# Performance work log

Measured on AMD Instinct MI355X. Metric: run time of the kernel, lower is better.

The kernel has to match this reference:

```python
import jax, jax.numpy as jnp
import numpy as np

SIGMA = 10.0
EPSILON = 46.0
BATCH = 4096
D_X = 1024
D_Y = 512


def setup_inputs() -> dict:
    key = jax.random.key(0)
    kx, ky = jax.random.split(key)
    x = jax.random.normal(kx, (BATCH, D_X), dtype=jnp.float32)
    y = jax.random.normal(ky, (BATCH, D_Y), dtype=jnp.float32)
    return {"x": x, "y": y}


def _pairwise_l2(a):
    # [B, B] matrix of ||a_i - a_j||_2 via the matmul trick; safe sqrt for grads.
    sq = jnp.sum(a * a, axis=-1)                      # [B]
    d2 = sq[:, None] + sq[None, :] - 2.0 * (a @ a.T)  # [B, B]
    d2 = jnp.maximum(d2, 0.0)
    return jnp.sqrt(jnp.where(d2 > 1e-12, d2, 1e-12))


def reference(x, y):
    b = x.shape[0]
    dx = _pairwise_l2(x)   # ||x_i - x_j||
    dy = _pairwise_l2(y)   # ||y_i - y_j||
    offdiag = 1.0 - jnp.eye(b, dtype=x.dtype)          # i != j
    mask = offdiag * (dx <= EPSILON).astype(x.dtype)   # threshold at epsilon
    w = jnp.exp(-dx / SIGMA)                           # heat-kernel weight
    loss = jnp.sum(mask * w * dy)
    return loss
```

## Files before the change

### kernel.cpp

```cpp
#include <hip/hip_runtime.h>
#include <hip/hip_bf16.h>
#include <hip/hip_fp8.h>
#include <stdint.h>

#define BATCH 4096
#define D_X   1024
#define D_Y   512

constexpr float SIGMA_INV = 0.1f;
constexpr float EPS_THR   = 46.0f;

constexpr int BMF   = 128;
constexpr int NTF   = BATCH / BMF;
constexpr int NBLKF = NTF * (NTF + 1) / 2;
constexpr int XS8   = D_X / 16;
constexpr int YS8   = D_Y / 16;

constexpr int BM = 128;
constexpr int NT = BATCH / BM;
constexpr int NBLK = NT * (NT + 1) / 2;

typedef __bf16 bf16x8 __attribute__((ext_vector_type(8)));
typedef float  f32x4  __attribute__((ext_vector_type(4)));
typedef unsigned short u16x8 __attribute__((ext_vector_type(8)));
typedef unsigned long long u64;
typedef u64 u64x2 __attribute__((ext_vector_type(2)));

__device__ __forceinline__ unsigned short f32_to_bf16_bits(float f) {
    unsigned int u = __builtin_bit_cast(unsigned int, f);
    unsigned int r = (u + 0x7FFFu + ((u >> 16) & 1u)) >> 16;
    return (unsigned short)r;
}

__device__ __forceinline__ int perm16(int u8) {
    int ks = u8 >> 2, kg = u8 & 3;
    return (ks >> 1) * 8 + kg * 2 + (ks & 1);
}

__global__ void __launch_bounds__(192)
convert_fp8(const float* __restrict__ x, const float* __restrict__ y,
            u64* __restrict__ xq, u64* __restrict__ yq,
            float* __restrict__ sqx, float* __restrict__ sqy) {
    __shared__ float part[2];
    const int row = blockIdx.x;
    const int t   = threadIdx.x;
    const int lane = t & 63;
    const int wid  = t >> 6;

    float nrm = 0.f;
    if (t < 128) {
        const float4* p = (const float4*)(x + (size_t)row * D_X + t * 8);
        float4 f0 = p[0], f1 = p[1];
        float e[8] = {f0.x, f0.y, f0.z, f0.w, f1.x, f1.y, f1.z, f1.w};
        u64 w = 0;
#pragma unroll
        for (int i = 0; i < 8; ++i) {
            __hip_fp8_e4m3 q(e[i]);
            float b = (float)q;
            nrm = fmaf(b, b, nrm);
            w |= (u64)q.__x << (8 * i);
        }
        xq[(size_t)row * 128 + (t & ~15) + perm16(t & 15)] = w;
    } else {
        int o = t - 128;
        const float4* p = (const float4*)(y + (size_t)row * D_Y + o * 8);
        float4 f0 = p[0], f1 = p[1];
        float e[8] = {f0.x, f0.y, f0.z, f0.w, f1.x, f1.y, f1.z, f1.w};
        u64 w = 0;
#pragma unroll
        for (int i = 0; i < 8; ++i) {
            __hip_fp8_e4m3 q(e[i]);
            float b = (float)q;
            nrm = fmaf(b, b, nrm);
            w |= (u64)q.__x << (8 * i);
        }
        yq[(size_t)row * 64 + (o & ~15) + perm16(o & 15)] = w;
    }
#pragma unroll
    for (int off = 32; off > 0; off >>= 1)
        nrm += __shfl_down(nrm, off, 64);
    if (lane == 0) {
        if (wid < 2) part[wid] = nrm;
        else         sqy[row] = nrm;
    }
    __syncthreads();
    if (t == 0) sqx[row] = part[0] + part[1];
}


__device__ __forceinline__ u64x2 ldsfrag2(const u16x8* T, int row, int c) {
    int slot = c ^ (row & 7);
    return __builtin_bit_cast(u64x2, T[row * 8 + slot]);
}

#define ISSUE(DST, BASE, OFF)                                              \
    {                                                                      \
        _Pragma("unroll")                                                  \
        for (int it = 0; it < 8; ++it)                                     \
            __builtin_amdgcn_global_load_lds(                              \
                (const uint32_t __attribute__((address_space(1)))*)(BASE[it] + (OFF)), \
                (uint32_t __attribute__((address_space(3)))*)((DST) + it * 256 + wid * 64), \
                16, 0, 0);                                                 \
    }

#define FRAGS_READ(BUF)                                                    \
        u64x2 fa[2][4], fb[2][4];                      \
        _Pragma("unroll")                                                  \
        for (int t2 = 0; t2 < 2; ++t2) {                                   \
            _Pragma("unroll")                                              \
            for (int m = 0; m < 4; ++m)                                    \
                fa[t2][m] = ldsfrag2(BUF, wr * 64 + m * 16 + lrow,         \
                                     t2 * 4 + kgrp);                       \
            _Pragma("unroll")                                              \
            for (int n = 0; n < 4; ++n)                                    \
                fb[t2][n] = ldsfrag2(BUF, 128 + wc * 64 + n * 16 + lrow,   \
                                     t2 * 4 + kgrp);                       \
        }

#define FRAGS_MFMA(ACC)                                                    \
        __builtin_amdgcn_s_setprio(1);                                     \
        _Pragma("unroll")                                                  \
        for (int t2 = 0; t2 < 2; ++t2)                                     \
            _Pragma("unroll")                                              \
            for (int h = 0; h < 2; ++h)                                    \
                _Pragma("unroll")                                          \
                for (int m = 0; m < 4; ++m)                                \
                    _Pragma("unroll")                                      \
                    for (int n = 0; n < 4; ++n)                            \
                        ACC[m][n] =                                        \
                            __builtin_amdgcn_mfma_f32_16x16x32_fp8_fp8(    \
                                (long)fa[t2][m][h], (long)fb[t2][n][h],    \
                                ACC[m][n], 0, 0, 0);                       \
        __builtin_amdgcn_s_setprio(0);

#define GSTEP(BUF, ACC, W, IBASE, IOFF)                                    \
    {                                                                      \
        asm volatile("s_waitcnt vmcnt(" #W ")" ::: "memory");              \
        __builtin_amdgcn_s_barrier();                                      \
        FRAGS_READ(BUF)                                                    \
        asm volatile("s_waitcnt lgkmcnt(0)" ::: "memory");                 \
        __builtin_amdgcn_s_barrier();                                      \
        ISSUE(BUF, IBASE, IOFF)                                            \
        FRAGS_MFMA(ACC)                                                    \
    }
#define GSTEP_NOISSUE(BUF, ACC, W)                                         \
    {                                                                      \
        asm volatile("s_waitcnt vmcnt(" #W ")" ::: "memory");              \
        __builtin_amdgcn_s_barrier();                                      \
        FRAGS_READ(BUF)                                                    \
        FRAGS_MFMA(ACC)                                                    \
    }

__global__ void __launch_bounds__(256, 2)
gram_fp8(const u16x8* __restrict__ xq, const u16x8* __restrict__ yq,
         const float* __restrict__ sqx, const float* __restrict__ sqy,
         float* __restrict__ out) {
    __shared__ u16x8 T0[2048], T1[2048];
    __shared__ float snxA[BMF], snxB[BMF], snyA[BMF], snyB[BMF];
    __shared__ float wsum[4];

    const int tid  = threadIdx.x;
    const int lane = tid & 63;
    const int wid  = tid >> 6;
    const int wr   = wid >> 1;
    const int wc   = wid & 1;
    const int lrow = lane & 15;
    const int kgrp = lane >> 4;

    int sb = (blockIdx.x & 7) * (NBLKF / 8) + (blockIdx.x >> 3);

    int t0 = sb, bi = 0;
    while (t0 >= NTF - bi) { t0 -= NTF - bi; ++bi; }
    const int bj = bi + t0;
    const int iA = bi * BMF;
    const int iB = bj * BMF;
    const bool diag = (bi == bj);

    if (tid < BMF) {
        snxA[tid] = sqx[iA + tid];
        snyA[tid] = sqy[iA + tid];
    } else {
        int u = tid - BMF;
        snxB[u] = sqx[iB + u];
        snyB[u] = sqy[iB + u];
    }

    const char* g[8];
#pragma unroll
    for (int it = 0; it < 8; ++it) {
        int ul   = it * 256 + wid * 64 + lane;
        int row  = ul >> 3;
        int st   = ul & 7;
        int lg   = st ^ (row & 7);
        int grow = (row < 128 ? iA + row : iB + row - 128);
        g[it] = (const char*)xq + (size_t)grow * (XS8 * 16) + lg * 16;
    }

    f32x4 accX[4][4] = {};
    f32x4 accY[4][4] = {};

    ISSUE(T0, g, 0)
    ISSUE(T1, g, 128)

    GSTEP(T0, accX, 8, g, 256)
    GSTEP(T1, accX, 8, g, 384)
    GSTEP(T0, accX, 8, g, 512)
    GSTEP(T1, accX, 8, g, 640)
    GSTEP(T0, accX, 8, g, 768)
    GSTEP(T1, accX, 8, g, 896)

#pragma unroll
    for (int it = 0; it < 8; ++it) {
        int ul   = it * 256 + wid * 64 + lane;
        int row  = ul >> 3;
        int st   = ul & 7;
        int lg   = st ^ (row & 7);
        int grow = (row < 128 ? iA + row : iB + row - 128);
        g[it] = (const char*)yq + (size_t)grow * (YS8 * 16) + lg * 16;
    }

    GSTEP(T0, accX, 8, g, 0)
    GSTEP(T1, accX, 8, g, 128)
    GSTEP(T0, accY, 8, g, 256)
    GSTEP(T1, accY, 8, g, 384)
    GSTEP_NOISSUE(T0, accY, 8)
    GSTEP_NOISSUE(T1, accY, 0)

    float local = 0.f;
#pragma unroll
    for (int m = 0; m < 4; ++m) {
#pragma unroll
        for (int n = 0; n < 4; ++n) {
            int col   = wc * 64 + n * 16 + lrow;
            float sxj = snxB[col];
            float syj = snyB[col];
#pragma unroll
            for (int r = 0; r < 4; ++r) {
                int rowi  = wr * 64 + m * 16 + kgrp * 4 + r;
                float d2x = snxA[rowi] + sxj - 2.f * accX[m][n][r];
                float dxv = sqrtf(fmaxf(d2x, 1e-12f));
                float d2y = snyA[rowi] + syj - 2.f * accY[m][n][r];
                float dyv = sqrtf(fmaxf(d2y, 1e-12f));
                int gi = iA + rowi, gj = iB + col;
                bool keep = (gi != gj) && (dxv <= EPS_THR);
                float contrib = __expf(-dxv * SIGMA_INV) * dyv;
                local += keep ? contrib : 0.f;
            }
        }
    }
    if (!diag) local *= 2.f;

#pragma unroll
    for (int off = 32; off > 0; off >>= 1)
        local += __shfl_down(local, off, 64);
    if (lane == 0) wsum[wid] = local;
    __syncthreads();
    if (tid == 0)
        atomicAdd(out, wsum[0] + wsum[1] + wsum[2] + wsum[3]);
}

__global__ void norms_kernel_fb(const float* __restrict__ x,
                                const float* __restrict__ y,
                                float* __restrict__ sqx,
                                float* __restrict__ sqy) {
    int row = blockIdx.x;
    int t   = threadIdx.x;
    const float4* xr = (const float4*)(x + (size_t)row * D_X);
    float sx = 0.f;
#pragma unroll
    for (int i = 0; i < D_X / 4 / 64; ++i) {
        float4 v = xr[t + i * 64];
        sx += v.x * v.x + v.y * v.y + v.z * v.z + v.w * v.w;
    }
    const float4* yr = (const float4*)(y + (size_t)row * D_Y);
    float sy = 0.f;
#pragma unroll
    for (int i = 0; i < D_Y / 4 / 64; ++i) {
        float4 v = yr[t + i * 64];
        sy += v.x * v.x + v.y * v.y + v.z * v.z + v.w * v.w;
    }
#pragma unroll
    for (int off = 32; off > 0; off >>= 1) {
        sx += __shfl_down(sx, off, 64);
        sy += __shfl_down(sy, off, 64);
    }
    if (t == 0) { sqx[row] = sx; sqy[row] = sy; }
}

__device__ __forceinline__ void stage_tile_fb(const float* __restrict__ src, int ld,
                                              int base_row, int k0,
                                              u16x8* __restrict__ dst, int tid) {
#pragma unroll
    for (int it = 0; it < 2; ++it) {
        int u   = tid + it * 256;
        int row = u >> 2;
        int q   = u & 3;
        const float4* p = (const float4*)(src + (size_t)(base_row + row) * ld + k0 + q * 16);
        float4 f0 = p[0], f1 = p[1], f2 = p[2], f3 = p[3];
        u16x8 lo, hi;
        lo[0] = f32_to_bf16_bits(f0.x); lo[1] = f32_to_bf16_bits(f0.y);
        lo[2] = f32_to_bf16_bits(f0.z); lo[3] = f32_to_bf16_bits(f0.w);
        lo[4] = f32_to_bf16_bits(f1.x); lo[5] = f32_to_bf16_bits(f1.y);
        lo[6] = f32_to_bf16_bits(f1.z); lo[7] = f32_to_bf16_bits(f1.w);
        hi[0] = f32_to_bf16_bits(f2.x); hi[1] = f32_to_bf16_bits(f2.y);
        hi[2] = f32_to_bf16_bits(f2.z); hi[3] = f32_to_bf16_bits(f2.w);
        hi[4] = f32_to_bf16_bits(f3.x); hi[5] = f32_to_bf16_bits(f3.y);
        hi[6] = f32_to_bf16_bits(f3.z); hi[7] = f32_to_bf16_bits(f3.w);
        int swz = row & 7;
        dst[row * 8 + ((2 * q) ^ swz)]     = lo;
        dst[row * 8 + ((2 * q + 1) ^ swz)] = hi;
    }
}

__device__ __forceinline__ void mfma16_fb(const bf16x8 a[4], const bf16x8 b[4],
                                          f32x4 acc[4][4]) {
#pragma unroll
    for (int m = 0; m < 4; ++m)
#pragma unroll
        for (int n = 0; n < 4; ++n)
            acc[m][n] = __builtin_amdgcn_mfma_f32_16x16x32_bf16(
                a[m], b[n], acc[m][n], 0, 0, 0);
}

__device__ __forceinline__ void load_frags_fb(const u16x8* As_, const u16x8* Bs_,
                                              int wr, int wc, int lrow, int kgrp,
                                              bf16x8 a[2][4], bf16x8 b[2][4]) {
#pragma unroll
    for (int ks = 0; ks < 2; ++ks) {
#pragma unroll
        for (int m = 0; m < 4; ++m) {
            int row  = wr * 64 + m * 16 + lrow;
            int slot = (ks * 4 + kgrp) ^ (row & 7);
            a[ks][m] = __builtin_bit_cast(bf16x8, As_[row * 8 + slot]);
        }
#pragma unroll
        for (int n = 0; n < 4; ++n) {
            int row  = wc * 64 + n * 16 + lrow;
            int slot = (ks * 4 + kgrp) ^ (row & 7);
            b[ks][n] = __builtin_bit_cast(bf16x8, Bs_[row * 8 + slot]);
        }
    }
}

__global__ void __launch_bounds__(256, 2)
graph_loss_fb(const float* __restrict__ x, const float* __restrict__ y,
              const float* __restrict__ sqx, const float* __restrict__ sqy,
              float* __restrict__ out) {
    __shared__ u16x8 As[BM * 8];
    __shared__ u16x8 Bs[BM * 8];
    __shared__ float snxA[BM], snxB[BM], snyA[BM], snyB[BM];
    __shared__ float wsum[4];

    const int tid  = threadIdx.x;
    const int lane = tid & 63;
    const int wid  = tid >> 6;
    const int wr   = wid >> 1;
    const int wc   = wid & 1;
    const int lrow = lane & 15;
    const int kgrp = lane >> 4;

    int t = blockIdx.x, bi = 0;
    while (t >= NT - bi) { t -= NT - bi; ++bi; }
    const int bj = bi + t;
    const int iA = bi * BM;
    const int iB = bj * BM;

    if (tid < BM) {
        snxA[tid] = sqx[iA + tid];
        snyA[tid] = sqy[iA + tid];
        snxB[tid] = sqx[iB + tid];
        snyB[tid] = sqy[iB + tid];
    }

    f32x4 accX[4][4] = {};
    f32x4 accY[4][4] = {};
    bf16x8 a[2][4], b[2][4];

    for (int kt = 0; kt < D_X / 64; ++kt) {
        __syncthreads();
        stage_tile_fb(x, D_X, iA, kt * 64, As, tid);
        stage_tile_fb(x, D_X, iB, kt * 64, Bs, tid);
        __syncthreads();
        load_frags_fb(As, Bs, wr, wc, lrow, kgrp, a, b);
#pragma unroll
        for (int ks = 0; ks < 2; ++ks) mfma16_fb(a[ks], b[ks], accX);
    }
    for (int kt = 0; kt < D_Y / 64; ++kt) {
        __syncthreads();
        stage_tile_fb(y, D_Y, iA, kt * 64, As, tid);
        stage_tile_fb(y, D_Y, iB, kt * 64, Bs, tid);
        __syncthreads();
        load_frags_fb(As, Bs, wr, wc, lrow, kgrp, a, b);
#pragma unroll
        for (int ks = 0; ks < 2; ++ks) mfma16_fb(a[ks], b[ks], accY);
    }

    float local = 0.f;
#pragma unroll
    for (int m = 0; m < 4; ++m) {
#pragma unroll
        for (int n = 0; n < 4; ++n) {
            int col   = wc * 64 + n * 16 + lrow;
            float sxj = snxB[col];
            float syj = snyB[col];
#pragma unroll
            for (int r = 0; r < 4; ++r) {
                int rowi  = wr * 64 + m * 16 + kgrp * 4 + r;
                float d2x = snxA[rowi] + sxj - 2.f * accX[m][n][r];
                float dxv = sqrtf(fmaxf(d2x, 1e-12f));
                float d2y = snyA[rowi] + syj - 2.f * accY[m][n][r];
                float dyv = sqrtf(fmaxf(d2y, 1e-12f));
                int gi = iA + rowi, gj = iB + col;
                bool keep = (gi != gj) && (dxv <= EPS_THR);
                float contrib = __expf(-dxv * SIGMA_INV) * dyv;
                local += keep ? contrib : 0.f;
            }
        }
    }
    if (bi != bj) local *= 2.f;

#pragma unroll
    for (int off = 32; off > 0; off >>= 1)
        local += __shfl_down(local, off, 64);
    if (lane == 0) wsum[wid] = local;
    __syncthreads();
    if (tid == 0)
        atomicAdd(out, wsum[0] + wsum[1] + wsum[2] + wsum[3]);
}

extern "C" void kernel_launch(void* const* d_in, const int* in_sizes, int n_in,
                              void* d_out, int out_size, void* d_ws, size_t ws_size,
                              hipStream_t stream) {
    const float* x = (const float*)d_in[0];
    const float* y = (const float*)d_in[1];
    float* out = (float*)d_out;

    hipMemsetAsync(d_out, 0, sizeof(float) * (size_t)out_size, stream);

    const size_t xq_bytes = (size_t)BATCH * D_X;
    const size_t yq_bytes = (size_t)BATCH * D_Y;
    const size_t sq_bytes = 2 * (size_t)BATCH * sizeof(float);
    const size_t need = xq_bytes + yq_bytes + sq_bytes;

    if (ws_size >= need) {
        u64*   xq  = (u64*)d_ws;
        u64*   yq  = (u64*)((char*)d_ws + xq_bytes);
        float* sqx = (float*)((char*)d_ws + xq_bytes + yq_bytes);
        float* sqy = sqx + BATCH;
        convert_fp8<<<BATCH, 192, 0, stream>>>(x, y, xq, yq, sqx, sqy);
        gram_fp8<<<NBLKF, 256, 0, stream>>>((const u16x8*)xq, (const u16x8*)yq,
                                            sqx, sqy, out);
    } else {
        float* sqx = (float*)d_ws;
        float* sqy = sqx + BATCH;
        norms_kernel_fb<<<BATCH, 64, 0, stream>>>(x, y, sqx, sqy);
        graph_loss_fb<<<NBLK, 256, 0, stream>>>(x, y, sqx, sqy, out);
    }
}
```

Before: 57.33 us.

## Pre-tile FP8 operands into fragment layout and load A fragments directly from global

The converter now writes FP8 data in a tiled, fragment-ordered layout, using an LDS transpose and atomically accumulated row norms. The Gram kernel reads the A-side fragments straight from global memory into registers, double-buffered one step ahead. Only the B tile now goes through LDS, which halves LDS traffic and async load count per step. The cost is an extra memset, LDS and global atomics for the norms, and A-side global loads that are not shared across waves and may add latency.

```diff
diff --git a/kernel.cpp b/kernel.cpp
--- a/kernel.cpp
+++ b/kernel.cpp
@@ -32,59 +32,65 @@
     return (unsigned short)r;
 }
 
-__device__ __forceinline__ int perm16(int u8) {
-    int ks = u8 >> 2, kg = u8 & 3;
-    return (ks >> 1) * 8 + kg * 2 + (ks & 1);
-}
-
-__global__ void __launch_bounds__(192)
-convert_fp8(const float* __restrict__ x, const float* __restrict__ y,
-            u64* __restrict__ xq, u64* __restrict__ yq,
-            float* __restrict__ sqx, float* __restrict__ sqy) {
-    __shared__ float part[2];
-    const int row = blockIdx.x;
+__device__ __forceinline__ int inv16(int pos) {
+    return (pos & 8) | ((pos >> 1) & 3) | ((pos & 1) << 2);
+}
+
+__global__ void __launch_bounds__(256)
+convert_ft(const float* __restrict__ x, const float* __restrict__ y,
+           u16x8* __restrict__ ftx, u16x8* __restrict__ fty,
+           float* __restrict__ sqx, float* __restrict__ sqy) {
+    __shared__ u16x8 L[64 * 16];
+    __shared__ float pn[64];
+    const int R   = blockIdx.x / 6;
+    const int seg = blockIdx.x % 6;
     const int t   = threadIdx.x;
-    const int lane = t & 63;
-    const int wid  = t >> 6;
-
-    float nrm = 0.f;
-    if (t < 128) {
-        const float4* p = (const float4*)(x + (size_t)row * D_X + t * 8);
-        float4 f0 = p[0], f1 = p[1];
-        float e[8] = {f0.x, f0.y, f0.z, f0.w, f1.x, f1.y, f1.z, f1.w};
-        u64 w = 0;
+    const bool isx = (seg < 4);
+    const int  cg  = isx ? seg : (seg - 4);
+    const float* src = isx ? x : y;
+    const int  ld  = isx ? D_X : D_Y;
+
+    if (t < 64) pn[t] = 0.f;
+    __syncthreads();
+
+#pragma unroll
+    for (int it = 0; it < 4; ++it) {
+        int idx = it * 256 + t;
+        int r = idx >> 4, jj = idx & 15;
+        int lc = cg * 16 + jj;
+        const float4* p = (const float4*)(src + (size_t)(R * 64 + r) * ld + lc * 16);
+        float4 f0 = p[0], f1 = p[1], f2 = p[2], f3 = p[3];
+        float e[16] = {f0.x, f0.y, f0.z, f0.w, f1.x, f1.y, f1.z, f1.w,
+                       f2.x, f2.y, f2.z, f2.w, f3.x, f3.y, f3.z, f3.w};
+        u16x8 v;
+        float part = 0.f;
 #pragma unroll
         for (int i = 0; i < 8; ++i) {
-            __hip_fp8_e4m3 q(e[i]);
-            float b = (float)q;
-            nrm = fmaf(b, b, nrm);
-            w |= (u64)q.__x << (8 * i);
+            __hip_fp8_e4m3 q0(e[2 * i]);
+            __hip_fp8_e4m3 q1(e[2 * i + 1]);
+            float b0 = (float)q0, b1 = (float)q1;
+            part = fmaf(b0, b0, part);
+            part = fmaf(b1, b1, part);
+            v[i] = (unsigned short)(q0.__x | ((unsigned short)q1.__x << 8));
         }
-        xq[(size_t)row * 128 + (t & ~15) + perm16(t & 15)] = w;
-    } else {
-        int o = t - 128;
-        const float4* p = (const float4*)(y + (size_t)row * D_Y + o * 8);
-        float4 f0 = p[0], f1 = p[1];
-        float e[8] = {f0.x, f0.y, f0.z, f0.w, f1.x, f1.y, f1.z, f1.w};
-        u64 w = 0;
-#pragma unroll
-        for (int i = 0; i < 8; ++i) {
-            __hip_fp8_e4m3 q(e[i]);
-            float b = (float)q;
-            nrm = fmaf(b, b, nrm);
-            w |= (u64)q.__x << (8 * i);
-        }
-        yq[(size_t)row * 64 + (o & ~15) + perm16(o & 15)] = w;
-    }
-#pragma unroll
-    for (int off = 32; off > 0; off >>= 1)
-        nrm += __shfl_down(nrm, off, 64);
-    if (lane == 0) {
-        if (wid < 2) part[wid] = nrm;
-        else         sqy[row] = nrm;
+        L[r * 16 + (jj ^ (r & 15))] = v;
+        atomicAdd(&pn[r], part);
     }
     __syncthreads();
-    if (t == 0) sqx[row] = part[0] + part[1];
+#pragma unroll
+    for (int it = 0; it < 4; ++it) {
+        int idx = it * 256 + t;
+        int scl = idx >> 6, r = idx & 63;
+        int sc  = cg * 16 + (it * 4 + (t >> 6));
+        (void)scl;
+        int lc  = (sc & ~15) | inv16(sc & 15);
+        int jj  = lc - cg * 16;
+        u16x8 v = L[r * 16 + (jj ^ (r & 15))];
+        if (isx) ftx[((size_t)R * XS8 + sc) * 64 + r] = v;
+        else     fty[((size_t)R * YS8 + sc) * 64 + r] = v;
+    }
+    __syncthreads();
+    if (t < 64) atomicAdd((isx ? sqx : sqy) + R * 64 + t, pn[t]);
 }
 
 
@@ -96,28 +102,28 @@
 #define ISSUE(DST, BASE, OFF)                                              \
     {                                                                      \
         _Pragma("unroll")                                                  \
-        for (int it = 0; it < 8; ++it)                                     \
+        for (int it = 0; it < 4; ++it)                                     \
             __builtin_amdgcn_global_load_lds(                              \
                 (const uint32_t __attribute__((address_space(1)))*)(BASE[it] + (OFF)), \
                 (uint32_t __attribute__((address_space(3)))*)((DST) + it * 256 + wid * 64), \
                 16, 0, 0);                                                 \
     }
 
-#define FRAGS_READ(BUF)                                                    \
-        u64x2 fa[2][4], fb[2][4];                      \
+#define AREAD(DST, APTR, AOFF)                                             \
+    _Pragma("unroll")                                                      \
+    for (int t2 = 0; t2 < 2; ++t2)                                         \
         _Pragma("unroll")                                                  \
-        for (int t2 = 0; t2 < 2; ++t2) {                                   \
-            _Pragma("unroll")                                              \
-            for (int m = 0; m < 4; ++m)                                    \
-                fa[t2][m] = ldsfrag2(BUF, wr * 64 + m * 16 + lrow,         \
-                                     t2 * 4 + kgrp);                       \
-            _Pragma("unroll")                                              \
-            for (int n = 0; n < 4; ++n)                                    \
-                fb[t2][n] = ldsfrag2(BUF, 128 + wc * 64 + n * 16 + lrow,   \
-                                     t2 * 4 + kgrp);                       \
-        }
-
-#define FRAGS_MFMA(ACC)                                                    \
+        for (int m = 0; m < 4; ++m)                                        \
+            DST[t2][m] = *(const u64x2*)((APTR) + (AOFF) + t2 * 4096 + m * 256);
+
+#define BREAD(FB, BUF)                                                     \
+    _Pragma("unroll")                                                      \
+    for (int t2 = 0; t2 < 2; ++t2)                                         \
+        _Pragma("unroll")                                                  \
+        for (int n = 0; n < 4; ++n)                                        \
+            FB[t2][n] = ldsfrag2(BUF, wc * 64 + n * 16 + lrow, t2 * 4 + kgrp);
+
+#define MFMA8(FA, FB, ACC)                                                 \
         __builtin_amdgcn_s_setprio(1);                                     \
         _Pragma("unroll")                                                  \
         for (int t2 = 0; t2 < 2; ++t2)                                     \
@@ -129,33 +135,45 @@
                     for (int n = 0; n < 4; ++n)                            \
                         ACC[m][n] =                                        \
                             __builtin_amdgcn_mfma_f32_16x16x32_fp8_fp8(    \
-                                (long)fa[t2][m][h], (long)fb[t2][n][h],    \
+                                (long)FA[t2][m][h], (long)FB[t2][n][h],    \
                                 ACC[m][n], 0, 0, 0);                       \
         __builtin_amdgcn_s_setprio(0);
 
-#define GSTEP(BUF, ACC, W, IBASE, IOFF)                                    \
+#define GSTEP(BUF, ACC, W, BOFF, FCUR, FNXT, APTR, AOFF)                   \
     {                                                                      \
         asm volatile("s_waitcnt vmcnt(" #W ")" ::: "memory");              \
         __builtin_amdgcn_s_barrier();                                      \
-        FRAGS_READ(BUF)                                                    \
+        u64x2 fb[2][4];                                                    \
+        BREAD(fb, BUF)                                                     \
+        AREAD(FNXT, APTR, AOFF)                                            \
         asm volatile("s_waitcnt lgkmcnt(0)" ::: "memory");                 \
         __builtin_amdgcn_s_barrier();                                      \
-        ISSUE(BUF, IBASE, IOFF)                                            \
-        FRAGS_MFMA(ACC)                                                    \
-    }
-#define GSTEP_NOISSUE(BUF, ACC, W)                                         \
+        ISSUE(BUF, g, BOFF)                                                \
+        MFMA8(FCUR, fb, ACC)                                               \
+    }
+#define GSTEP_NIR(BUF, ACC, W, FCUR, FNXT, APTR, AOFF)                     \
     {                                                                      \
         asm volatile("s_waitcnt vmcnt(" #W ")" ::: "memory");              \
         __builtin_amdgcn_s_barrier();                                      \
-        FRAGS_READ(BUF)                                                    \
-        FRAGS_MFMA(ACC)                                                    \
+        u64x2 fb[2][4];                                                    \
+        BREAD(fb, BUF)                                                     \
+        AREAD(FNXT, APTR, AOFF)                                            \
+        MFMA8(FCUR, fb, ACC)                                               \
+    }
+#define GSTEP_NI(BUF, ACC, W, FCUR)                                        \
+    {                                                                      \
+        asm volatile("s_waitcnt vmcnt(" #W ")" ::: "memory");              \
+        __builtin_amdgcn_s_barrier();                                      \
+        u64x2 fb[2][4];                                                    \
+        BREAD(fb, BUF)                                                     \
+        MFMA8(FCUR, fb, ACC)                                               \
     }
 
 __global__ void __launch_bounds__(256, 2)
-gram_fp8(const u16x8* __restrict__ xq, const u16x8* __restrict__ yq,
+gram_fp8(const u16x8* __restrict__ ftx, const u16x8* __restrict__ fty,
          const float* __restrict__ sqx, const float* __restrict__ sqy,
          float* __restrict__ out) {
-    __shared__ u16x8 T0[2048], T1[2048];
+    __shared__ u16x8 B0[1024], B1[1024];
     __shared__ float snxA[BMF], snxB[BMF], snyA[BMF], snyB[BMF];
     __shared__ float wsum[4];
 
@@ -185,46 +203,48 @@
         snyB[u] = sqy[iB + u];
     }
 
-    const char* g[8];
-#pragma unroll
-    for (int it = 0; it < 8; ++it) {
-        int ul   = it * 256 + wid * 64 + lane;
-        int row  = ul >> 3;
-        int st   = ul & 7;
-        int lg   = st ^ (row & 7);
-        int grow = (row < 128 ? iA + row : iB + row - 128);
-        g[it] = (const char*)xq + (size_t)grow * (XS8 * 16) + lg * 16;
-    }
+    const char* g[4];
+#pragma unroll
+    for (int it = 0; it < 4; ++it) {
+        int ul = it * 256 + wid * 64 + lane;
+        int rr = ul >> 3, st = ul & 7;
+        int lg = st ^ (rr & 7);
+        g[it] = (const char*)ftx +
+                (((size_t)(iB / 64 + (rr >> 6)) * XS8 + lg) * 64 + (rr & 63)) * 16;
+    }
+    const char* Ax = (const char*)ftx +
+        (((size_t)(iA / 64 + wr) * XS8 + kgrp) * 64 + lrow) * 16;
+    const char* Ay = (const char*)fty +
+        (((size_t)(iA / 64 + wr) * YS8 + kgrp) * 64 + lrow) * 16;
 
     f32x4 accX[4][4] = {};
     f32x4 accY[4][4] = {};
-
-    ISSUE(T0, g, 0)
-    ISSUE(T1, g, 128)
-
-    GSTEP(T0, accX, 8, g, 256)
-    GSTEP(T1, accX, 8, g, 384)
-    GSTEP(T0, accX, 8, g, 512)
-    GSTEP(T1, accX, 8, g, 640)
-    GSTEP(T0, accX, 8, g, 768)
-    GSTEP(T1, accX, 8, g, 896)
-
-#pragma unroll
-    for (int it = 0; it < 8; ++it) {
-        int ul   = it * 256 + wid * 64 + lane;
-        int row  = ul >> 3;
-        int st   = ul & 7;
-        int lg   = st ^ (row & 7);
-        int grow = (row < 128 ? iA + row : iB + row - 128);
-        g[it] = (const char*)yq + (size_t)grow * (YS8 * 16) + lg * 16;
-    }
-
-    GSTEP(T0, accX, 8, g, 0)
-    GSTEP(T1, accX, 8, g, 128)
-    GSTEP(T0, accY, 8, g, 256)
-    GSTEP(T1, accY, 8, g, 384)
-    GSTEP_NOISSUE(T0, accY, 8)
-    GSTEP_NOISSUE(T1, accY, 0)
+    u64x2 fa0[2][4], fa1[2][4];
+
+    ISSUE(B0, g, 0)
+    ISSUE(B1, g, 8192)
+    AREAD(fa0, Ax, 0)
+
+    GSTEP(B0, accX, 4, 2 * 8192, fa0, fa1, Ax, 1 * 8192)
+    GSTEP(B1, accX, 4, 3 * 8192, fa1, fa0, Ax, 2 * 8192)
+    GSTEP(B0, accX, 4, 4 * 8192, fa0, fa1, Ax, 3 * 8192)
+    GSTEP(B1, accX, 4, 5 * 8192, fa1, fa0, Ax, 4 * 8192)
+    GSTEP(B0, accX, 4, 6 * 8192, fa0, fa1, Ax, 5 * 8192)
+    GSTEP(B1, accX, 4, 7 * 8192, fa1, fa0, Ax, 6 * 8192)
+#pragma unroll
+    for (int it = 0; it < 4; ++it) {
+        int ul = it * 256 + wid * 64 + lane;
+        int rr = ul >> 3, st = ul & 7;
+        int lg = st ^ (rr & 7);
+        g[it] = (const char*)fty +
+                (((size_t)(iB / 64 + (rr >> 6)) * YS8 + lg) * 64 + (rr & 63)) * 16;
+    }
+    GSTEP(B0, accX, 4, 0,        fa0, fa1, Ax, 7 * 8192)
+    GSTEP(B1, accX, 4, 1 * 8192, fa1, fa0, Ay, 0)
+    GSTEP(B0, accY, 4, 2 * 8192, fa0, fa1, Ay, 1 * 8192)
+    GSTEP(B1, accY, 4, 3 * 8192, fa1, fa0, Ay, 2 * 8192)
+    GSTEP_NIR(B0, accY, 4, fa0, fa1, Ay, 3 * 8192)
+    GSTEP_NI(B1, accY, 0, fa1)
 
     float local = 0.f;
 #pragma unroll
@@ -437,19 +457,19 @@
 
     hipMemsetAsync(d_out, 0, sizeof(float) * (size_t)out_size, stream);
 
-    const size_t xq_bytes = (size_t)BATCH * D_X;
-    const size_t yq_bytes = (size_t)BATCH * D_Y;
-    const size_t sq_bytes = 2 * (size_t)BATCH * sizeof(float);
-    const size_t need = xq_bytes + yq_bytes + sq_bytes;
+    const size_t ftx_bytes = (size_t)BATCH * D_X;
+    const size_t fty_bytes = (size_t)BATCH * D_Y;
+    const size_t sq_bytes  = 2 * (size_t)BATCH * sizeof(float);
+    const size_t need = ftx_bytes + fty_bytes + sq_bytes;
 
     if (ws_size >= need) {
-        u64*   xq  = (u64*)d_ws;
-        u64*   yq  = (u64*)((char*)d_ws + xq_bytes);
-        float* sqx = (float*)((char*)d_ws + xq_bytes + yq_bytes);
+        u16x8* ftx = (u16x8*)d_ws;
+        u16x8* fty = (u16x8*)((char*)d_ws + ftx_bytes);
+        float* sqx = (float*)((char*)d_ws + ftx_bytes + fty_bytes);
         float* sqy = sqx + BATCH;
-        convert_fp8<<<BATCH, 192, 0, stream>>>(x, y, xq, yq, sqx, sqy);
-        gram_fp8<<<NBLKF, 256, 0, stream>>>((const u16x8*)xq, (const u16x8*)yq,
-                                            sqx, sqy, out);
+        hipMemsetAsync(sqx, 0, sq_bytes, stream);
+        convert_ft<<<64 * 6, 256, 0, stream>>>(x, y, ftx, fty, sqx, sqy);
+        gram_fp8<<<NBLKF, 256, 0, stream>>>(ftx, fty, sqx, sqy, out);
     } else {
         float* sqx = (float*)d_ws;
         float* sqy = sqx + BATCH;
```

Measured after the change: 68.52 us. 1.2x slower.

## Switch gram kernel to triple-buffered 64-byte K slices with one barrier per step

Applied to the files above, without the earlier changes.

Replaces the double-buffered 128-byte K-slice pipeline with three 64-byte-wide LDS buffers rotated in a ring. The second barrier and the lgkmcnt wait before reissuing global-to-LDS loads go away, because the buffer being written is never the one being read. The aim is more overlap between loads, LDS reads and MFMA work. The cost is twice as many pipeline steps and barriers, fewer MFMAs per step, and a narrower 4-way XOR swizzle that may cause more LDS bank conflicts.

```diff
diff --git a/kernel.cpp b/kernel.cpp
--- a/kernel.cpp
+++ b/kernel.cpp
@@ -88,74 +88,78 @@
 }
 
 
-__device__ __forceinline__ u64x2 ldsfrag2(const u16x8* T, int row, int c) {
-    int slot = c ^ (row & 7);
-    return __builtin_bit_cast(u64x2, T[row * 8 + slot]);
+__device__ __forceinline__ u64x2 ldsfrag4(const u16x8* T, int row, int kg) {
+    return __builtin_bit_cast(u64x2, T[row * 4 + (kg ^ (row & 3))]);
 }
 
 #define ISSUE(DST, BASE, OFF)                                              \
     {                                                                      \
         _Pragma("unroll")                                                  \
-        for (int it = 0; it < 8; ++it)                                     \
+        for (int it = 0; it < 4; ++it)                                     \
             __builtin_amdgcn_global_load_lds(                              \
                 (const uint32_t __attribute__((address_space(1)))*)(BASE[it] + (OFF)), \
                 (uint32_t __attribute__((address_space(3)))*)((DST) + it * 256 + wid * 64), \
                 16, 0, 0);                                                 \
     }
 
-#define FRAGS_READ(BUF)                                                    \
-        u64x2 fa[2][4], fb[2][4];                      \
-        _Pragma("unroll")                                                  \
-        for (int t2 = 0; t2 < 2; ++t2) {                                   \
+#define MFMA_BLK(FA, FB, ACC)                                              \
+        __builtin_amdgcn_s_setprio(1);                                     \
+        _Pragma("unroll")                                                  \
+        for (int h = 0; h < 2; ++h)                                        \
             _Pragma("unroll")                                              \
             for (int m = 0; m < 4; ++m)                                    \
-                fa[t2][m] = ldsfrag2(BUF, wr * 64 + m * 16 + lrow,         \
-                                     t2 * 4 + kgrp);                       \
-            _Pragma("unroll")                                              \
-            for (int n = 0; n < 4; ++n)                                    \
-                fb[t2][n] = ldsfrag2(BUF, 128 + wc * 64 + n * 16 + lrow,   \
-                                     t2 * 4 + kgrp);                       \
-        }
-
-#define FRAGS_MFMA(ACC)                                                    \
-        __builtin_amdgcn_s_setprio(1);                                     \
-        _Pragma("unroll")                                                  \
-        for (int t2 = 0; t2 < 2; ++t2)                                     \
-            _Pragma("unroll")                                              \
-            for (int h = 0; h < 2; ++h)                                    \
                 _Pragma("unroll")                                          \
-                for (int m = 0; m < 4; ++m)                                \
-                    _Pragma("unroll")                                      \
-                    for (int n = 0; n < 4; ++n)                            \
-                        ACC[m][n] =                                        \
-                            __builtin_amdgcn_mfma_f32_16x16x32_fp8_fp8(    \
-                                (long)fa[t2][m][h], (long)fb[t2][n][h],    \
-                                ACC[m][n], 0, 0, 0);                       \
+                for (int n = 0; n < 4; ++n)                                \
+                    ACC[m][n] = __builtin_amdgcn_mfma_f32_16x16x32_fp8_fp8(\
+                        (long)FA[m][h], (long)FB[n][h], ACC[m][n], 0,0,0); \
         __builtin_amdgcn_s_setprio(0);
 
-#define GSTEP(BUF, ACC, W, IBASE, IOFF)                                    \
+#define GS(RB, WB, GSRC, GOFF, ACC)                                        \
     {                                                                      \
-        asm volatile("s_waitcnt vmcnt(" #W ")" ::: "memory");              \
+        asm volatile("s_waitcnt vmcnt(4)" ::: "memory");                   \
         __builtin_amdgcn_s_barrier();                                      \
-        FRAGS_READ(BUF)                                                    \
-        asm volatile("s_waitcnt lgkmcnt(0)" ::: "memory");                 \
+        u64x2 fa[4], fb[4];                                                \
+        _Pragma("unroll")                                                  \
+        for (int m = 0; m < 4; ++m)                                        \
+            fa[m] = ldsfrag4(RB, wr * 64 + m * 16 + lrow, kgrp);           \
+        _Pragma("unroll")                                                  \
+        for (int n = 0; n < 4; ++n)                                        \
+            fb[n] = ldsfrag4(RB, 128 + wc * 64 + n * 16 + lrow, kgrp);     \
+        ISSUE(WB, GSRC, GOFF)                                              \
+        MFMA_BLK(fa, fb, ACC)                                              \
+    }
+#define GS_NI4(RB, ACC)                                                    \
+    {                                                                      \
+        asm volatile("s_waitcnt vmcnt(4)" ::: "memory");                   \
         __builtin_amdgcn_s_barrier();                                      \
-        ISSUE(BUF, IBASE, IOFF)                                            \
-        FRAGS_MFMA(ACC)                                                    \
-    }
-#define GSTEP_NOISSUE(BUF, ACC, W)                                         \
+        u64x2 fa[4], fb[4];                                                \
+        _Pragma("unroll")                                                  \
+        for (int m = 0; m < 4; ++m)                                        \
+            fa[m] = ldsfrag4(RB, wr * 64 + m * 16 + lrow, kgrp);           \
+        _Pragma("unroll")                                                  \
+        for (int n = 0; n < 4; ++n)                                        \
+            fb[n] = ldsfrag4(RB, 128 + wc * 64 + n * 16 + lrow, kgrp);     \
+        MFMA_BLK(fa, fb, ACC)                                              \
+    }
+#define GS_NI0(RB, ACC)                                                    \
     {                                                                      \
-        asm volatile("s_waitcnt vmcnt(" #W ")" ::: "memory");              \
+        asm volatile("s_waitcnt vmcnt(0)" ::: "memory");                   \
         __builtin_amdgcn_s_barrier();                                      \
-        FRAGS_READ(BUF)                                                    \
-        FRAGS_MFMA(ACC)                                                    \
+        u64x2 fa[4], fb[4];                                                \
+        _Pragma("unroll")                                                  \
+        for (int m = 0; m < 4; ++m)                                        \
+            fa[m] = ldsfrag4(RB, wr * 64 + m * 16 + lrow, kgrp);           \
+        _Pragma("unroll")                                                  \
+        for (int n = 0; n < 4; ++n)                                        \
+            fb[n] = ldsfrag4(RB, 128 + wc * 64 + n * 16 + lrow, kgrp);     \
+        MFMA_BLK(fa, fb, ACC)                                              \
     }
 
 __global__ void __launch_bounds__(256, 2)
 gram_fp8(const u16x8* __restrict__ xq, const u16x8* __restrict__ yq,
          const float* __restrict__ sqx, const float* __restrict__ sqy,
          float* __restrict__ out) {
-    __shared__ u16x8 T0[2048], T1[2048];
+    __shared__ u16x8 B0[1024], B1[1024], B2[1024];
     __shared__ float snxA[BMF], snxB[BMF], snyA[BMF], snyB[BMF];
     __shared__ float wsum[4];
 
@@ -185,46 +189,49 @@
         snyB[u] = sqy[iB + u];
     }
 
-    const char* g[8];
-#pragma unroll
-    for (int it = 0; it < 8; ++it) {
+    const char* gx[4];
+    const char* gy[4];
+#pragma unroll
+    for (int it = 0; it < 4; ++it) {
         int ul   = it * 256 + wid * 64 + lane;
-        int row  = ul >> 3;
-        int st   = ul & 7;
-        int lg   = st ^ (row & 7);
+        int row  = ul >> 2;
+        int st   = ul & 3;
+        int lg   = st ^ (row & 3);
         int grow = (row < 128 ? iA + row : iB + row - 128);
-        g[it] = (const char*)xq + (size_t)grow * (XS8 * 16) + lg * 16;
+        gx[it] = (const char*)xq + (size_t)grow * (XS8 * 16) + lg * 16;
+        gy[it] = (const char*)yq + (size_t)grow * (YS8 * 16) + lg * 16;
     }
 
     f32x4 accX[4][4] = {};
     f32x4 accY[4][4] = {};
 
-    ISSUE(T0, g, 0)
-    ISSUE(T1, g, 128)
-
-    GSTEP(T0, accX, 8, g, 256)
-    GSTEP(T1, accX, 8, g, 384)
-    GSTEP(T0, accX, 8, g, 512)
-    GSTEP(T1, accX, 8, g, 640)
-    GSTEP(T0, accX, 8, g, 768)
-    GSTEP(T1, accX, 8, g, 896)
-
-#pragma unroll
-    for (int it = 0; it < 8; ++it) {
-        int ul   = it * 256 + wid * 64 + lane;
-        int row  = ul >> 3;
-        int st   = ul & 7;
-        int lg   = st ^ (row & 7);
-        int grow = (row < 128 ? iA + row : iB + row - 128);
-        g[it] = (const char*)yq + (size_t)grow * (YS8 * 16) + lg * 16;
-    }
-
-    GSTEP(T0, accX, 8, g, 0)
-    GSTEP(T1, accX, 8, g, 128)
-    GSTEP(T0, accY, 8, g, 256)
-    GSTEP(T1, accY, 8, g, 384)
-    GSTEP_NOISSUE(T0, accY, 8)
-    GSTEP_NOISSUE(T1, accY, 0)
+    ISSUE(B0, gx, 0)
+    ISSUE(B1, gx, 64)
+
+    GS(B0, B2, gx, 128, accX)
+    GS(B1, B0, gx, 192, accX)
+    GS(B2, B1, gx, 256, accX)
+    GS(B0, B2, gx, 320, accX)
+    GS(B1, B0, gx, 384, accX)
+    GS(B2, B1, gx, 448, accX)
+    GS(B0, B2, gx, 512, accX)
+    GS(B1, B0, gx, 576, accX)
+    GS(B2, B1, gx, 640, accX)
+    GS(B0, B2, gx, 704, accX)
+    GS(B1, B0, gx, 768, accX)
+    GS(B2, B1, gx, 832, accX)
+    GS(B0, B2, gx, 896, accX)
+    GS(B1, B0, gx, 960, accX)
+    GS(B2, B1, gy, 0,   accX)
+    GS(B0, B2, gy, 64,  accX)
+    GS(B1, B0, gy, 128, accY)
+    GS(B2, B1, gy, 192, accY)
+    GS(B0, B2, gy, 256, accY)
+    GS(B1, B0, gy, 320, accY)
+    GS(B2, B1, gy, 384, accY)
+    GS(B0, B2, gy, 448, accY)
+    GS_NI4(B1, accY)
+    GS_NI0(B2, accY)
 
     float local = 0.f;
 #pragma unroll
```

Measured after the change: 59.31 us. 3.5% more time.

## Double the K-step depth per LDS stage in fp8 gram kernel

Applied to the files above, without the earlier changes.

Each pipeline stage now loads 256 bytes of K per row instead of 128, which doubles the LDS buffers to 64KB each and halves the number of barrier/wait steps. Global address generation is simplified to four base pointers plus row strides, replacing per-iteration pointer arrays. Occupancy drops from two blocks per CU to one because of the larger LDS footprint and register usage. The intent is to cut synchronization overhead and give more MFMA work per stage, with the risk that losing the second resident block exposes load latency.

```diff
diff --git a/kernel.cpp b/kernel.cpp
--- a/kernel.cpp
+++ b/kernel.cpp
@@ -15,6 +15,8 @@
 constexpr int NBLKF = NTF * (NTF + 1) / 2;
 constexpr int XS8   = D_X / 16;
 constexpr int YS8   = D_Y / 16;
+constexpr int XRB   = XS8 * 16;
+constexpr int YRB   = YS8 * 16;
 
 constexpr int BM = 128;
 constexpr int NT = BATCH / BM;
@@ -88,39 +90,40 @@
 }
 
 
-__device__ __forceinline__ u64x2 ldsfrag2(const u16x8* T, int row, int c) {
-    int slot = c ^ (row & 7);
-    return __builtin_bit_cast(u64x2, T[row * 8 + slot]);
-}
-
-#define ISSUE(DST, BASE, OFF)                                              \
+__device__ __forceinline__ u64x2 ldsfragN(const u16x8* T, int row, int t2, int kgrp) {
+    int c = ((t2 >> 1) << 3) | (((t2 & 1) * 4 + kgrp) ^ (row & 7));
+    return __builtin_bit_cast(u64x2, T[row * 16 + c]);
+}
+
+#define ISSUE(DST, AX, BX, RS16, OFF)                                      \
     {                                                                      \
         _Pragma("unroll")                                                  \
-        for (int it = 0; it < 8; ++it)                                     \
+        for (int it = 0; it < 16; ++it) {                                  \
+            const char* bp = (it < 8) ? ((AX) + it * (RS16))               \
+                                      : ((BX) + (it - 8) * (RS16));        \
             __builtin_amdgcn_global_load_lds(                              \
-                (const uint32_t __attribute__((address_space(1)))*)(BASE[it] + (OFF)), \
+                (const uint32_t __attribute__((address_space(1)))*)(bp + (OFF)), \
                 (uint32_t __attribute__((address_space(3)))*)((DST) + it * 256 + wid * 64), \
                 16, 0, 0);                                                 \
+        }                                                                  \
     }
 
 #define FRAGS_READ(BUF)                                                    \
-        u64x2 fa[2][4], fb[2][4];                      \
+        u64x2 fa[4][4], fb[4][4];                          \
         _Pragma("unroll")                                                  \
-        for (int t2 = 0; t2 < 2; ++t2) {                                   \
+        for (int t2 = 0; t2 < 4; ++t2) {                                   \
             _Pragma("unroll")                                              \
             for (int m = 0; m < 4; ++m)                                    \
-                fa[t2][m] = ldsfrag2(BUF, wr * 64 + m * 16 + lrow,         \
-                                     t2 * 4 + kgrp);                       \
+                fa[t2][m] = ldsfragN(BUF, wr * 64 + m * 16 + lrow, t2, kgrp); \
             _Pragma("unroll")                                              \
             for (int n = 0; n < 4; ++n)                                    \
-                fb[t2][n] = ldsfrag2(BUF, 128 + wc * 64 + n * 16 + lrow,   \
-                                     t2 * 4 + kgrp);                       \
+                fb[t2][n] = ldsfragN(BUF, 128 + wc * 64 + n * 16 + lrow, t2, kgrp); \
         }
 
 #define FRAGS_MFMA(ACC)                                                    \
         __builtin_amdgcn_s_setprio(1);                                     \
         _Pragma("unroll")                                                  \
-        for (int t2 = 0; t2 < 2; ++t2)                                     \
+        for (int t2 = 0; t2 < 4; ++t2)                                     \
             _Pragma("unroll")                                              \
             for (int h = 0; h < 2; ++h)                                    \
                 _Pragma("unroll")                                          \
@@ -133,17 +136,17 @@
                                 ACC[m][n], 0, 0, 0);                       \
         __builtin_amdgcn_s_setprio(0);
 
-#define GSTEP(BUF, ACC, W, IBASE, IOFF)                                    \
+#define GSTEP(BUF, ACC, W, AX, BX, RS16, OFF)                              \
     {                                                                      \
         asm volatile("s_waitcnt vmcnt(" #W ")" ::: "memory");              \
         __builtin_amdgcn_s_barrier();                                      \
         FRAGS_READ(BUF)                                                    \
         asm volatile("s_waitcnt lgkmcnt(0)" ::: "memory");                 \
         __builtin_amdgcn_s_barrier();                                      \
-        ISSUE(BUF, IBASE, IOFF)                                            \
+        ISSUE(BUF, AX, BX, RS16, OFF)                                      \
         FRAGS_MFMA(ACC)                                                    \
     }
-#define GSTEP_NOISSUE(BUF, ACC, W)                                         \
+#define GSTEP_NI(BUF, ACC, W)                                              \
     {                                                                      \
         asm volatile("s_waitcnt vmcnt(" #W ")" ::: "memory");              \
         __builtin_amdgcn_s_barrier();                                      \
@@ -151,11 +154,11 @@
         FRAGS_MFMA(ACC)                                                    \
     }
 
-__global__ void __launch_bounds__(256, 2)
+__global__ void __launch_bounds__(256, 1)
 gram_fp8(const u16x8* __restrict__ xq, const u16x8* __restrict__ yq,
          const float* __restrict__ sqx, const float* __restrict__ sqy,
          float* __restrict__ out) {
-    __shared__ u16x8 T0[2048], T1[2048];
+    __shared__ u16x8 T0[4096], T1[4096];
     __shared__ float snxA[BMF], snxB[BMF], snyA[BMF], snyB[BMF];
     __shared__ float wsum[4];
 
@@ -185,46 +188,27 @@
         snyB[u] = sqy[iB + u];
     }
 
-    const char* g[8];
-#pragma unroll
-    for (int it = 0; it < 8; ++it) {
-        int ul   = it * 256 + wid * 64 + lane;
-        int row  = ul >> 3;
-        int st   = ul & 7;
-        int lg   = st ^ (row & 7);
-        int grow = (row < 128 ? iA + row : iB + row - 128);
-        g[it] = (const char*)xq + (size_t)grow * (XS8 * 16) + lg * 16;
-    }
+    const int r0 = tid >> 4;
+    const int h0 = (tid >> 3) & 1;
+    const int lg = (tid & 7) ^ (r0 & 7);
+    const int cb = (h0 * 8 + lg) * 16;
+    const char* gxA = (const char*)xq + (size_t)(iA + r0) * XRB + cb;
+    const char* gxB = (const char*)xq + (size_t)(iB + r0) * XRB + cb;
+    const char* gyA = (const char*)yq + (size_t)(iA + r0) * YRB + cb;
+    const char* gyB = (const char*)yq + (size_t)(iB + r0) * YRB + cb;
 
     f32x4 accX[4][4] = {};
     f32x4 accY[4][4] = {};
 
-    ISSUE(T0, g, 0)
-    ISSUE(T1, g, 128)
-
-    GSTEP(T0, accX, 8, g, 256)
-    GSTEP(T1, accX, 8, g, 384)
-    GSTEP(T0, accX, 8, g, 512)
-    GSTEP(T1, accX, 8, g, 640)
-    GSTEP(T0, accX, 8, g, 768)
-    GSTEP(T1, accX, 8, g, 896)
-
-#pragma unroll
-    for (int it = 0; it < 8; ++it) {
-        int ul   = it * 256 + wid * 64 + lane;
-        int row  = ul >> 3;
-        int st   = ul & 7;
-        int lg   = st ^ (row & 7);
-        int grow = (row < 128 ? iA + row : iB + row - 128);
-        g[it] = (const char*)yq + (size_t)grow * (YS8 * 16) + lg * 16;
-    }
-
-    GSTEP(T0, accX, 8, g, 0)
-    GSTEP(T1, accX, 8, g, 128)
-    GSTEP(T0, accY, 8, g, 256)
-    GSTEP(T1, accY, 8, g, 384)
-    GSTEP_NOISSUE(T0, accY, 8)
-    GSTEP_NOISSUE(T1, accY, 0)
+    ISSUE(T0, gxA, gxB, 16 * XRB, 0)
+    ISSUE(T1, gxA, gxB, 16 * XRB, 256)
+
+    GSTEP(T0, accX, 16, gxA, gxB, 16 * XRB, 512)
+    GSTEP(T1, accX, 16, gxA, gxB, 16 * XRB, 768)
+    GSTEP(T0, accX, 16, gyA, gyB, 16 * YRB, 0)
+    GSTEP(T1, accX, 16, gyA, gyB, 16 * YRB, 256)
+    GSTEP_NI(T0, accY, 16)
+    GSTEP_NI(T1, accY, 0)
 
     float local = 0.f;
 #pragma unroll
```

After: 75.47 us. 31.6% more time.
